# Kernel tuning notes

Measured on AMD Instinct MI355X. Metric: run time of the kernel, lower is better.

## Reference

```python
import jax, jax.numpy as jnp
import numpy as np

TOPK = 8


def setup_inputs() -> dict:
    key = jax.random.key(0)
    k1, k2 = jax.random.split(key)
    tokens, dim, n_experts = 16384, 7168, 256
    x = jax.random.normal(k1, (tokens, dim), dtype=jnp.float32)
    # xavier_uniform-ish scale for router weight
    limit = (6.0 / (n_experts + dim)) ** 0.5
    weight = jax.random.uniform(k2, (n_experts, dim), dtype=jnp.float32,
                                minval=-limit, maxval=limit)
    return {"x": x, "weight": weight}


def reference(x, weight):
    # logits: [tokens, n_experts] = x @ weight.T
    logits = jnp.einsum('td,ed->te', x, weight)
    scores = jax.nn.softmax(logits, axis=-1)
    # torch.topk returns values & indices; gather(scores, 1, indices) == values
    weights, indices = jax.lax.top_k(scores, TOPK)
    return weights, indices
```

## Files before the change

### kernel.cpp

```cpp
#include <hip/hip_runtime.h>
#include <math.h>

#define TOKENS 16384
#define DIM    7168
#define NEXP   256
#define TK     8
#define BM     64
#define BK     32
#define NKT    (DIM / BK)
#define DELTA  8.0e-3f
#define MAXC   12

#define XOFF(b) ((b) * 2048)
#define WOFF(b) (4096 + (b) * 8192)
#define K1_LDS_BYTES 81920

#define WS_CAND 0
#define WS_CNT  (TOKENS * 16 * 4)
#define WS_M    (WS_CNT + TOKENS * 4)
#define WS_INVS (WS_M + TOKENS * 4)

__device__ __forceinline__ void gload16(const float* g, float* l) {
    __builtin_amdgcn_global_load_lds(
        (const __attribute__((address_space(1))) void*)g,
        (__attribute__((address_space(3))) void*)l, 16, 0, 0);
}

__global__ __launch_bounds__(256)
void gate_gemm(const float* __restrict__ x, const float* __restrict__ w,
               int* __restrict__ wsCand, int* __restrict__ wsCnt,
               float* __restrict__ wsM, float* __restrict__ wsInvs)
{
    extern __shared__ __align__(16) float smem[];
    const int t    = threadIdx.x;
    const int tx   = t & 31;
    const int ty   = t >> 5;
    const int lane = t & 63;
    const int wv   = t >> 6;
    const int tok0 = blockIdx.x * BM;

    const int kpart = lane & 7;
    const int xsub  = lane >> 3;

#define STAGE(kt, buf) do {                                             \
    _Pragma("unroll")                                                   \
    for (int u = 0; u < 2; ++u) {                                       \
        const int row = (wv * 2 + u) * 8 + xsub;                        \
        gload16(x + (size_t)(tok0 + row) * DIM + (kt) * BK + kpart * 4, \
                smem + XOFF(buf) + (wv * 2 + u) * 256);                 \
    }                                                                   \
    _Pragma("unroll")                                                   \
    for (int v = 0; v < 8; ++v) {                                       \
        const int c  = wv * 8 + v;                                      \
        const int kg = c >> 2, eb = c & 3;                              \
        gload16(w + (size_t)(eb * 64 + lane) * DIM + (kt) * BK + kg * 4,\
                smem + WOFF(buf) + kg * 1024 + eb * 256);               \
    }                                                                   \
} while (0)

    float acc[8][8];
    #pragma unroll
    for (int i = 0; i < 8; ++i)
        #pragma unroll
        for (int j = 0; j < 8; ++j)
            acc[i][j] = 0.0f;

    STAGE(0, 0);
    __syncthreads();

    for (int kt = 0; kt < NKT; ++kt) {
        const int cur = kt & 1;
        if (kt + 1 < NKT) STAGE(kt + 1, cur ^ 1);
        const float* Xb = smem + XOFF(cur) + ty * 8 * 32;
        const float* Wb = smem + WOFF(cur) + tx * 4;
        #pragma unroll
        for (int kg = 0; kg < 8; ++kg) {
            float4 xf[8];
            #pragma unroll
            for (int i = 0; i < 8; ++i)
                xf[i] = *(const float4*)(Xb + i * 32 + kg * 4);
            #pragma unroll
            for (int j = 0; j < 8; ++j) {
                float4 wf = *(const float4*)(Wb + kg * 1024 + j * 128);
                #pragma unroll
                for (int i = 0; i < 8; ++i) {
                    acc[i][j] = fmaf(xf[i].x, wf.x, acc[i][j]);
                    acc[i][j] = fmaf(xf[i].y, wf.y, acc[i][j]);
                    acc[i][j] = fmaf(xf[i].z, wf.z, acc[i][j]);
                    acc[i][j] = fmaf(xf[i].w, wf.w, acc[i][j]);
                }
            }
        }
        __syncthreads();
    }

    float* lgf = smem;
    #pragma unroll
    for (int i = 0; i < 8; ++i)
        #pragma unroll
        for (int j = 0; j < 8; ++j)
            lgf[(ty * 8 + i) * 260 + tx + 32 * j] = acc[i][j];
    __syncthreads();

    for (int r16 = 0; r16 < 16; ++r16) {
        const int row  = wv * 16 + r16;
        const int gtok = tok0 + row;
        float4 v = *(const float4*)(lgf + (size_t)row * 260 + lane * 4);
        float vv[4] = {v.x, v.y, v.z, v.w};

        float m = fmaxf(fmaxf(vv[0], vv[1]), fmaxf(vv[2], vv[3]));
        #pragma unroll
        for (int off = 32; off >= 1; off >>= 1)
            m = fmaxf(m, __shfl_xor(m, off));

        float s = expf(vv[0] - m) + expf(vv[1] - m)
                + expf(vv[2] - m) + expf(vv[3] - m);
        #pragma unroll
        for (int off = 32; off >= 1; off >>= 1)
            s += __shfl_xor(s, off);

        int   taken = 0;
        int   ncand = 0;
        float s8    = 0.0f;
        int   my_ci = 1 << 30;
        for (int it = 0; it < MAXC; ++it) {
            float bv = -INFINITY;
            int   bi = 1 << 30;
            #pragma unroll
            for (int j = 0; j < 4; ++j) {
                float cv = ((taken >> j) & 1) ? -INFINITY : vv[j];
                int   ci = lane * 4 + j;
                if (cv > bv || (cv == bv && ci < bi)) { bv = cv; bi = ci; }
            }
            #pragma unroll
            for (int off = 32; off >= 1; off >>= 1) {
                float ov = __shfl_xor(bv, off);
                int   oi = __shfl_xor(bi, off);
                if (ov > bv || (ov == bv && oi < bi)) { bv = ov; bi = oi; }
            }
            if (it == 7) s8 = bv;
            if (it >= 8 && bv < s8 - DELTA) break;
            if (lane == it) my_ci = bi;
            if ((bi >> 2) == lane) taken |= 1 << (bi & 3);
            ncand = it + 1;
        }

        if (lane < ncand) wsCand[gtok * 16 + lane] = my_ci;
        if (lane == 0) {
            wsCnt[gtok]  = ncand;
            wsM[gtok]    = m;
            wsInvs[gtok] = 1.0f / s;
        }
    }
}

__global__ __launch_bounds__(64, 1)
void gate_repair(const float* __restrict__ x,
                 const float* __restrict__ w,
                 const int* __restrict__ wsCand,
                 const int* __restrict__ wsCnt,
                 const float* __restrict__ wsM,
                 const float* __restrict__ wsInvs,
                 float* __restrict__ outw,
                 float* __restrict__ outi)
{
    const int lane = threadIdx.x;
    const int gtok = blockIdx.x;

    const int   nc   = wsCnt[gtok];
    const float m    = wsM[gtok];
    const float invs = wsInvs[gtok];
    int my_ci = (lane < nc) ? wsCand[gtok * 16 + lane] : (1 << 30);

    const float* xrow = x + (size_t)gtok * DIM + lane * 4;
    float4 xv[28];
    #pragma unroll
    for (int j = 0; j < 28; ++j)
        xv[j] = *(const float4*)(xrow + j * 256);

    double ev = -1.0e300;
    for (int c = 0; c < nc; ++c) {
        const int e = __shfl(my_ci, c);
        const float* wrow = w + (size_t)e * DIM + lane * 4;
        double a0 = 0.0, a1 = 0.0, a2 = 0.0, a3 = 0.0;
        #pragma unroll
        for (int j = 0; j < 28; j += 4) {
            float4 q0 = *(const float4*)(wrow + (j + 0) * 256);
            float4 q1 = *(const float4*)(wrow + (j + 1) * 256);
            float4 q2 = *(const float4*)(wrow + (j + 2) * 256);
            float4 q3 = *(const float4*)(wrow + (j + 3) * 256);
            a0 = fma((double)xv[j + 0].x, (double)q0.x, a0);
            a0 = fma((double)xv[j + 0].y, (double)q0.y, a0);
            a0 = fma((double)xv[j + 0].z, (double)q0.z, a0);
            a0 = fma((double)xv[j + 0].w, (double)q0.w, a0);
            a1 = fma((double)xv[j + 1].x, (double)q1.x, a1);
            a1 = fma((double)xv[j + 1].y, (double)q1.y, a1);
            a1 = fma((double)xv[j + 1].z, (double)q1.z, a1);
            a1 = fma((double)xv[j + 1].w, (double)q1.w, a1);
            a2 = fma((double)xv[j + 2].x, (double)q2.x, a2);
            a2 = fma((double)xv[j + 2].y, (double)q2.y, a2);
            a2 = fma((double)xv[j + 2].z, (double)q2.z, a2);
            a2 = fma((double)xv[j + 2].w, (double)q2.w, a2);
            a3 = fma((double)xv[j + 3].x, (double)q3.x, a3);
            a3 = fma((double)xv[j + 3].y, (double)q3.y, a3);
            a3 = fma((double)xv[j + 3].z, (double)q3.z, a3);
            a3 = fma((double)xv[j + 3].w, (double)q3.w, a3);
        }
        double tot = (a0 + a1) + (a2 + a3);
        #pragma unroll
        for (int off = 32; off >= 1; off >>= 1)
            tot += __shfl_xor(tot, off);
        if (lane == c) ev = tot;
    }

    for (int it = 0; it < TK; ++it) {
        double bv2 = ev;
        int    bi2 = my_ci;
        int    bs2 = lane;
        #pragma unroll
        for (int off = 32; off >= 1; off >>= 1) {
            double ov = __shfl_xor(bv2, off);
            int    oi = __shfl_xor(bi2, off);
            int    os = __shfl_xor(bs2, off);
            if (ov > bv2 || (ov == bv2 && oi < bi2)) {
                bv2 = ov; bi2 = oi; bs2 = os;
            }
        }
        if (lane == it) {
            outw[(size_t)gtok * TK + it] = expf((float)bv2 - m) * invs;
            outi[(size_t)gtok * TK + it] = (float)bi2;
        }
        if (lane == bs2) ev = -1.0e300;
    }
}

extern "C" void kernel_launch(void* const* d_in, const int* in_sizes, int n_in,
                              void* d_out, int out_size, void* d_ws, size_t ws_size,
                              hipStream_t stream) {
    const float* x = (const float*)d_in[0];
    const float* w = (const float*)d_in[1];
    float* outw = (float*)d_out;
    float* outi = outw + (size_t)TOKENS * TK;
    char* wsb = (char*)d_ws;
    int*   wsCand = (int*)(wsb + WS_CAND);
    int*   wsCnt  = (int*)(wsb + WS_CNT);
    float* wsM    = (float*)(wsb + WS_M);
    float* wsInvs = (float*)(wsb + WS_INVS);

    gate_gemm<<<dim3(TOKENS / BM), dim3(256), K1_LDS_BYTES, stream>>>(
        x, w, wsCand, wsCnt, wsM, wsInvs);
    gate_repair<<<dim3(TOKENS), dim3(64), 0, stream>>>(
        x, w, wsCand, wsCnt, wsM, wsInvs, outw, outi);
}
```

Baseline: 1.850 ms.

## Double threads per GEMM block and do softmax/top-k from registers

Raises the gate GEMM block from 256 to 512 threads, halving each thread's accumulator tile to 4x8 so register pressure drops and two blocks may fit per CU. The staging loads are split across the extra waves. The epilogue no longer writes logits to LDS and re-reads them. Each half-wave of 32 lanes now runs softmax and candidate top-k directly on its register rows using 32-lane shuffles. In exchange, each thread loads more W from LDS per FMA, and the per-token reductions now run as four sequential rows per half-wave.

```diff
diff --git a/kernel.cpp b/kernel.cpp
--- a/kernel.cpp
+++ b/kernel.cpp
@@ -26,7 +26,7 @@
         (__attribute__((address_space(3))) void*)l, 16, 0, 0);
 }
 
-__global__ __launch_bounds__(256)
+__global__ __launch_bounds__(512, 2)
 void gate_gemm(const float* __restrict__ x, const float* __restrict__ w,
                int* __restrict__ wsCand, int* __restrict__ wsCnt,
                float* __restrict__ wsM, float* __restrict__ wsInvs)
@@ -39,28 +39,22 @@
     const int wv   = t >> 6;
     const int tok0 = blockIdx.x * BM;
 
-    const int kpart = lane & 7;
-    const int xsub  = lane >> 3;
-
-#define STAGE(kt, buf) do {                                             \
-    _Pragma("unroll")                                                   \
-    for (int u = 0; u < 2; ++u) {                                       \
-        const int row = (wv * 2 + u) * 8 + xsub;                        \
-        gload16(x + (size_t)(tok0 + row) * DIM + (kt) * BK + kpart * 4, \
-                smem + XOFF(buf) + (wv * 2 + u) * 256);                 \
-    }                                                                   \
-    _Pragma("unroll")                                                   \
-    for (int v = 0; v < 8; ++v) {                                       \
-        const int c  = wv * 8 + v;                                      \
-        const int kg = c >> 2, eb = c & 3;                              \
-        gload16(w + (size_t)(eb * 64 + lane) * DIM + (kt) * BK + kg * 4,\
-                smem + WOFF(buf) + kg * 1024 + eb * 256);               \
-    }                                                                   \
+#define STAGE(kt, buf) do {                                               \
+    gload16(x + (size_t)(tok0 + wv * 8 + (lane >> 3)) * DIM               \
+                + (kt) * BK + (lane & 7) * 4,                             \
+            smem + XOFF(buf) + wv * 256);                                 \
+    _Pragma("unroll")                                                     \
+    for (int v = 0; v < 4; ++v) {                                         \
+        const int c  = wv * 4 + v;                                        \
+        const int kg = c >> 2, eb = c & 3;                                \
+        gload16(w + (size_t)(eb * 64 + lane) * DIM + (kt) * BK + kg * 4,  \
+                smem + WOFF(buf) + kg * 1024 + eb * 256);                 \
+    }                                                                     \
 } while (0)
 
-    float acc[8][8];
+    float acc[4][8];
     #pragma unroll
-    for (int i = 0; i < 8; ++i)
+    for (int i = 0; i < 4; ++i)
         #pragma unroll
         for (int j = 0; j < 8; ++j)
             acc[i][j] = 0.0f;
@@ -71,19 +65,19 @@
     for (int kt = 0; kt < NKT; ++kt) {
         const int cur = kt & 1;
         if (kt + 1 < NKT) STAGE(kt + 1, cur ^ 1);
-        const float* Xb = smem + XOFF(cur) + ty * 8 * 32;
+        const float* Xb = smem + XOFF(cur) + ty * 4 * 32;
         const float* Wb = smem + WOFF(cur) + tx * 4;
         #pragma unroll
         for (int kg = 0; kg < 8; ++kg) {
-            float4 xf[8];
-            #pragma unroll
-            for (int i = 0; i < 8; ++i)
+            float4 xf[4];
+            #pragma unroll
+            for (int i = 0; i < 4; ++i)
                 xf[i] = *(const float4*)(Xb + i * 32 + kg * 4);
             #pragma unroll
             for (int j = 0; j < 8; ++j) {
                 float4 wf = *(const float4*)(Wb + kg * 1024 + j * 128);
                 #pragma unroll
-                for (int i = 0; i < 8; ++i) {
+                for (int i = 0; i < 4; ++i) {
                     acc[i][j] = fmaf(xf[i].x, wf.x, acc[i][j]);
                     acc[i][j] = fmaf(xf[i].y, wf.y, acc[i][j]);
                     acc[i][j] = fmaf(xf[i].z, wf.z, acc[i][j]);
@@ -94,29 +88,25 @@
         __syncthreads();
     }
 
-    float* lgf = smem;
-    #pragma unroll
-    for (int i = 0; i < 8; ++i)
-        #pragma unroll
-        for (int j = 0; j < 8; ++j)
-            lgf[(ty * 8 + i) * 260 + tx + 32 * j] = acc[i][j];
-    __syncthreads();
-
-    for (int r16 = 0; r16 < 16; ++r16) {
-        const int row  = wv * 16 + r16;
-        const int gtok = tok0 + row;
-        float4 v = *(const float4*)(lgf + (size_t)row * 260 + lane * 4);
-        float vv[4] = {v.x, v.y, v.z, v.w};
-
-        float m = fmaxf(fmaxf(vv[0], vv[1]), fmaxf(vv[2], vv[3]));
-        #pragma unroll
-        for (int off = 32; off >= 1; off >>= 1)
+    const int hl = lane & 31;
+    for (int i = 0; i < 4; ++i) {
+        const int gtok = tok0 + ty * 4 + i;
+        float vv[8];
+        #pragma unroll
+        for (int j = 0; j < 8; ++j) vv[j] = acc[i][j];
+
+        float m = vv[0];
+        #pragma unroll
+        for (int j = 1; j < 8; ++j) m = fmaxf(m, vv[j]);
+        #pragma unroll
+        for (int off = 16; off >= 1; off >>= 1)
             m = fmaxf(m, __shfl_xor(m, off));
 
-        float s = expf(vv[0] - m) + expf(vv[1] - m)
-                + expf(vv[2] - m) + expf(vv[3] - m);
-        #pragma unroll
-        for (int off = 32; off >= 1; off >>= 1)
+        float s = 0.0f;
+        #pragma unroll
+        for (int j = 0; j < 8; ++j) s += expf(vv[j] - m);
+        #pragma unroll
+        for (int off = 16; off >= 1; off >>= 1)
             s += __shfl_xor(s, off);
 
         int   taken = 0;
@@ -127,26 +117,26 @@
             float bv = -INFINITY;
             int   bi = 1 << 30;
             #pragma unroll
-            for (int j = 0; j < 4; ++j) {
+            for (int j = 0; j < 8; ++j) {
                 float cv = ((taken >> j) & 1) ? -INFINITY : vv[j];
-                int   ci = lane * 4 + j;
+                int   ci = 32 * j + tx;
                 if (cv > bv || (cv == bv && ci < bi)) { bv = cv; bi = ci; }
             }
             #pragma unroll
-            for (int off = 32; off >= 1; off >>= 1) {
+            for (int off = 16; off >= 1; off >>= 1) {
                 float ov = __shfl_xor(bv, off);
                 int   oi = __shfl_xor(bi, off);
                 if (ov > bv || (ov == bv && oi < bi)) { bv = ov; bi = oi; }
             }
             if (it == 7) s8 = bv;
             if (it >= 8 && bv < s8 - DELTA) break;
-            if (lane == it) my_ci = bi;
-            if ((bi >> 2) == lane) taken |= 1 << (bi & 3);
+            if (hl == it) my_ci = bi;
+            if ((bi & 31) == hl) taken |= 1 << (bi >> 5);
             ncand = it + 1;
         }
 
-        if (lane < ncand) wsCand[gtok * 16 + lane] = my_ci;
-        if (lane == 0) {
+        if (hl < ncand) wsCand[gtok * 16 + hl] = my_ci;
+        if (hl == 0) {
             wsCnt[gtok]  = ncand;
             wsM[gtok]    = m;
             wsInvs[gtok] = 1.0f / s;
@@ -247,7 +237,7 @@
     float* wsM    = (float*)(wsb + WS_M);
     float* wsInvs = (float*)(wsb + WS_INVS);
 
-    gate_gemm<<<dim3(TOKENS / BM), dim3(256), K1_LDS_BYTES, stream>>>(
+    gate_gemm<<<dim3(TOKENS / BM), dim3(512), K1_LDS_BYTES, stream>>>(
         x, w, wsCand, wsCnt, wsM, wsInvs);
     gate_repair<<<dim3(TOKENS), dim3(64), 0, stream>>>(
         x, w, wsCand, wsCnt, wsM, wsInvs, outw, outi);
```

Result: faster. 1.571 ms (-15.1%).
